# Kernel optimization log

Measured on AMD Instinct MI355X. Metric: run time of the kernel, lower is better.

## Reference

```python
import jax, jax.numpy as jnp
import numpy as np

ALPHA = 0.7
BETTA = 0.3
EPS = 1e-8


def _unit(v):
    n = jnp.linalg.norm(v, axis=-1, keepdims=True)
    return v / jnp.where(n > 0, n, 1.0)


def setup_inputs() -> dict:
    key = jax.random.key(0)
    k1, k2 = jax.random.split(key)
    N, D = 2097152, 3
    vec_1 = jax.random.normal(k1, (N, D), dtype=jnp.float32)
    vec_2 = jax.random.normal(k2, (N, D), dtype=jnp.float32)
    return {"vec_1": vec_1, "vec_2": vec_2}


def reference(vec_1, vec_2):
    # Row mask: keep rows where ||vec_1|| > 1e-8. Instead of boolean gather
    # (data-dependent shape), weight rows by the mask and divide by the count.
    norm1 = jnp.linalg.norm(vec_1, axis=-1, keepdims=True)  # [N,1]
    mask = (norm1 > EPS).astype(vec_1.dtype)                # [N,1]

    n1 = _unit(vec_1)                                       # [N,3]
    u2 = _unit(vec_2)
    # angle between vec_1 and vec_2 (RotationVectors.angle)
    cos_sim = jnp.clip(jnp.sum(n1 * u2, axis=-1), -1.0, 1.0)  # [N]
    a = jnp.arccos(cos_sim)
    # orthonormal companion: Gram-Schmidt of vec_2 against n1
    n2 = _unit(vec_2 - n1 * jnp.sum(n1 * vec_2, axis=-1, keepdims=True))

    sin_a = jnp.sin(a)[:, None]            # [N,1]
    cos_a_m1 = (jnp.cos(a) - 1.0)[:, None]  # [N,1]

    # bmm(M, ones) is just the row-sum of M. For M = x yT the row-sum is
    # x * sum(y), so we never materialize the [N,3,3] outer products:
    s1 = jnp.sum(n1, axis=-1, keepdims=True)  # [N,1]
    s2 = jnp.sum(n2, axis=-1, keepdims=True)
    u_ta = sin_a * (n2 * s1 - n1 * s2)        # transform_a @ ones, [N,3]
    u_tb = cos_a_m1 * (n1 * s1 + n2 * s2)     # transform_b @ ones, [N,3]
    # I @ ones == ones, so mse(I@ones, ones) == 0 elementwise.
    per_row = ALPHA * u_ta ** 2 + BETTA * u_tb ** 2  # [N,3]

    cnt = jnp.maximum(jnp.sum(mask), 1.0)
    loss = jnp.sum(per_row * mask, axis=0) / cnt     # mean over kept rows -> [3]
    return jnp.nan_to_num(loss, nan=0.0, posinf=0.1, neginf=-0.1)
```

## Files before the change

### kernel.cpp

```cpp
#include <hip/hip_runtime.h>
#include <math.h>

#define ALPHA 0.7f
#define BETTA 0.3f
#define EPS   1e-8f

#define BLOCK 256
#define ROWS_PER_THREAD 4
#define TILE_ROWS (BLOCK * ROWS_PER_THREAD)
#define TILE_F4   (TILE_ROWS * 3 / 4)

__device__ __forceinline__ void row_contrib(float x1, float y1, float z1,
                                            float x2, float y2, float z2,
                                            float& a0, float& a1, float& a2,
                                            float& ac) {
    float q1 = x1 * x1 + y1 * y1 + z1 * z1;
    float m = (q1 > EPS * EPS) ? 1.0f : 0.0f;
    float inv1 = (q1 > 0.0f) ? rsqrtf(q1) : 0.0f;
    float n1x = x1 * inv1, n1y = y1 * inv1, n1z = z1 * inv1;

    float q2 = x2 * x2 + y2 * y2 + z2 * z2;
    float inv2 = (q2 > 0.0f) ? rsqrtf(q2) : 0.0f;
    float u2x = x2 * inv2, u2y = y2 * inv2, u2z = z2 * inv2;

    float c = n1x * u2x + n1y * u2y + n1z * u2z;
    c = fminf(1.0f, fmaxf(-1.0f, c));
    float sin_a = sqrtf(fmaxf(0.0f, 1.0f - c * c));
    float cm1 = c - 1.0f;

    float d = n1x * x2 + n1y * y2 + n1z * z2;
    float wx = x2 - n1x * d, wy = y2 - n1y * d, wz = z2 - n1z * d;
    float wq = wx * wx + wy * wy + wz * wz;
    float invw = (wq > 0.0f) ? rsqrtf(wq) : 0.0f;
    float n2x = wx * invw, n2y = wy * invw, n2z = wz * invw;

    float s1 = n1x + n1y + n1z;
    float s2 = n2x + n2y + n2z;

    float tax = sin_a * (n2x * s1 - n1x * s2);
    float tay = sin_a * (n2y * s1 - n1y * s2);
    float taz = sin_a * (n2z * s1 - n1z * s2);

    float tbx = cm1 * (n1x * s1 + n2x * s2);
    float tby = cm1 * (n1y * s1 + n2y * s2);
    float tbz = cm1 * (n1z * s1 + n2z * s2);

    a0 += (ALPHA * tax * tax + BETTA * tbx * tbx) * m;
    a1 += (ALPHA * tay * tay + BETTA * tby * tby) * m;
    a2 += (ALPHA * taz * taz + BETTA * tbz * tbz) * m;
    ac += m;
}

__global__ __launch_bounds__(BLOCK) void trl_reduce(const float* __restrict__ v1,
                                                    const float* __restrict__ v2,
                                                    float4* __restrict__ ws,
                                                    int n_rows) {
    __shared__ float4 ldsA[TILE_F4];
    __shared__ float4 ldsB[TILE_F4];

    int t = threadIdx.x;
    long tile_row0 = (long)blockIdx.x * TILE_ROWS;

    float a0 = 0.0f, a1 = 0.0f, a2 = 0.0f, ac = 0.0f;

    if (tile_row0 + TILE_ROWS <= n_rows) {
        const float4* g1 = (const float4*)v1;
        const float4* g2 = (const float4*)v2;
        long base = (long)blockIdx.x * TILE_F4;

        float4 la0 = g1[base + 0 * BLOCK + t];
        float4 la1 = g1[base + 1 * BLOCK + t];
        float4 la2 = g1[base + 2 * BLOCK + t];
        float4 lb0 = g2[base + 0 * BLOCK + t];
        float4 lb1 = g2[base + 1 * BLOCK + t];
        float4 lb2 = g2[base + 2 * BLOCK + t];

        ldsA[0 * BLOCK + t] = la0;
        ldsA[1 * BLOCK + t] = la1;
        ldsA[2 * BLOCK + t] = la2;
        ldsB[0 * BLOCK + t] = lb0;
        ldsB[1 * BLOCK + t] = lb1;
        ldsB[2 * BLOCK + t] = lb2;
        __syncthreads();

        float4 A0 = ldsA[3 * t + 0];
        float4 A1 = ldsA[3 * t + 1];
        float4 A2 = ldsA[3 * t + 2];
        float4 B0 = ldsB[3 * t + 0];
        float4 B1 = ldsB[3 * t + 1];
        float4 B2 = ldsB[3 * t + 2];

        row_contrib(A0.x, A0.y, A0.z, B0.x, B0.y, B0.z, a0, a1, a2, ac);
        row_contrib(A0.w, A1.x, A1.y, B0.w, B1.x, B1.y, a0, a1, a2, ac);
        row_contrib(A1.z, A1.w, A2.x, B1.z, B1.w, B2.x, a0, a1, a2, ac);
        row_contrib(A2.y, A2.z, A2.w, B2.y, B2.z, B2.w, a0, a1, a2, ac);
    } else {
        long row0 = tile_row0 + (long)t * ROWS_PER_THREAD;
        for (long r = row0; r < n_rows && r < row0 + ROWS_PER_THREAD; ++r) {
            const float* q1 = v1 + r * 3;
            const float* q2 = v2 + r * 3;
            row_contrib(q1[0], q1[1], q1[2], q2[0], q2[1], q2[2], a0, a1, a2, ac);
        }
    }

    for (int off = 32; off > 0; off >>= 1) {
        a0 += __shfl_down(a0, off, 64);
        a1 += __shfl_down(a1, off, 64);
        a2 += __shfl_down(a2, off, 64);
        ac += __shfl_down(ac, off, 64);
    }

    __shared__ float smem[4][4];
    int lane = t & 63;
    int wave = t >> 6;
    if (lane == 0) {
        smem[wave][0] = a0;
        smem[wave][1] = a1;
        smem[wave][2] = a2;
        smem[wave][3] = ac;
    }
    __syncthreads();
    if (t == 0) {
        float4 o;
        o.x = smem[0][0] + smem[1][0] + smem[2][0] + smem[3][0];
        o.y = smem[0][1] + smem[1][1] + smem[2][1] + smem[3][1];
        o.z = smem[0][2] + smem[1][2] + smem[2][2] + smem[3][2];
        o.w = smem[0][3] + smem[1][3] + smem[2][3] + smem[3][3];
        ws[blockIdx.x] = o;
    }
}

__global__ __launch_bounds__(256) void trl_final(const float4* __restrict__ ws,
                                                 float* __restrict__ out,
                                                 int nblocks) {
    float s0 = 0.0f, s1 = 0.0f, s2 = 0.0f, sc = 0.0f;
    for (int i = threadIdx.x; i < nblocks; i += 256) {
        float4 p = ws[i];
        s0 += p.x; s1 += p.y; s2 += p.z; sc += p.w;
    }
    for (int off = 32; off > 0; off >>= 1) {
        s0 += __shfl_down(s0, off, 64);
        s1 += __shfl_down(s1, off, 64);
        s2 += __shfl_down(s2, off, 64);
        sc += __shfl_down(sc, off, 64);
    }
    __shared__ float smem[4][4];
    int lane = threadIdx.x & 63;
    int wave = threadIdx.x >> 6;
    if (lane == 0) {
        smem[wave][0] = s0;
        smem[wave][1] = s1;
        smem[wave][2] = s2;
        smem[wave][3] = sc;
    }
    __syncthreads();
    if (threadIdx.x < 3) {
        float num = smem[0][threadIdx.x] + smem[1][threadIdx.x] +
                    smem[2][threadIdx.x] + smem[3][threadIdx.x];
        float cnt = smem[0][3] + smem[1][3] + smem[2][3] + smem[3][3];
        cnt = fmaxf(cnt, 1.0f);
        float v = num / cnt;
        if (isnan(v)) v = 0.0f;
        else if (isinf(v)) v = (v > 0.0f) ? 0.1f : -0.1f;
        out[threadIdx.x] = v;
    }
}

extern "C" void kernel_launch(void* const* d_in, const int* in_sizes, int n_in,
                              void* d_out, int out_size, void* d_ws, size_t ws_size,
                              hipStream_t stream) {
    const float* v1 = (const float*)d_in[0];
    const float* v2 = (const float*)d_in[1];
    float* out = (float*)d_out;
    float4* ws = (float4*)d_ws;

    int n_rows = in_sizes[0] / 3;

    int grid = (n_rows + TILE_ROWS - 1) / TILE_ROWS;

    trl_reduce<<<grid, BLOCK, 0, stream>>>(v1, v2, ws, n_rows);
    trl_final<<<1, 256, 0, stream>>>(ws, out, grid);
}
```

Before: 89.87 us.

## Use persistent blocks with double-buffered LDS tiles and register prefetch

Replaces the one-tile-per-block grid (2048 blocks) with a fixed grid of up to 512 blocks. Each block walks a contiguous range of tiles and prefetches the next tile into registers while the current tile is computed from a double-buffered LDS staging area. The aim is to hide global load latency and to cut the number of partial sums the final kernel has to reduce. In exchange, far fewer waves are in flight per CU to cover memory latency, and any tail rows are handled serially by block 0.

```diff
diff --git a/kernel.cpp b/kernel.cpp
--- a/kernel.cpp
+++ b/kernel.cpp
@@ -6,9 +6,10 @@
 #define EPS   1e-8f
 
 #define BLOCK 256
-#define ROWS_PER_THREAD 4
-#define TILE_ROWS (BLOCK * ROWS_PER_THREAD)
+#define RPT   4
+#define TILE_ROWS (BLOCK * RPT)
 #define TILE_F4   (TILE_ROWS * 3 / 4)
+#define NBLOCKS 512
 
 __device__ __forceinline__ void row_contrib(float x1, float y1, float z1,
                                             float x2, float y2, float z2,
@@ -54,49 +55,72 @@
 __global__ __launch_bounds__(BLOCK) void trl_reduce(const float* __restrict__ v1,
                                                     const float* __restrict__ v2,
                                                     float4* __restrict__ ws,
-                                                    int n_rows) {
-    __shared__ float4 ldsA[TILE_F4];
-    __shared__ float4 ldsB[TILE_F4];
+                                                    int n_rows, int n_tiles,
+                                                    int iters) {
+    __shared__ float4 ldsA[2][TILE_F4];
+    __shared__ float4 ldsB[2][TILE_F4];
+    __shared__ float smem[4][4];
 
     int t = threadIdx.x;
-    long tile_row0 = (long)blockIdx.x * TILE_ROWS;
+    const float4* g1 = (const float4*)v1;
+    const float4* g2 = (const float4*)v2;
+
+    long tile0 = (long)blockIdx.x * iters;
+    int my_tiles = 0;
+    if (tile0 < n_tiles) {
+        long rem = (long)n_tiles - tile0;
+        my_tiles = (rem < iters) ? (int)rem : iters;
+    }
 
     float a0 = 0.0f, a1 = 0.0f, a2 = 0.0f, ac = 0.0f;
-
-    if (tile_row0 + TILE_ROWS <= n_rows) {
-        const float4* g1 = (const float4*)v1;
-        const float4* g2 = (const float4*)v2;
-        long base = (long)blockIdx.x * TILE_F4;
-
-        float4 la0 = g1[base + 0 * BLOCK + t];
-        float4 la1 = g1[base + 1 * BLOCK + t];
-        float4 la2 = g1[base + 2 * BLOCK + t];
-        float4 lb0 = g2[base + 0 * BLOCK + t];
-        float4 lb1 = g2[base + 1 * BLOCK + t];
-        float4 lb2 = g2[base + 2 * BLOCK + t];
-
-        ldsA[0 * BLOCK + t] = la0;
-        ldsA[1 * BLOCK + t] = la1;
-        ldsA[2 * BLOCK + t] = la2;
-        ldsB[0 * BLOCK + t] = lb0;
-        ldsB[1 * BLOCK + t] = lb1;
-        ldsB[2 * BLOCK + t] = lb2;
+    float4 ra[3], rb[3];
+
+    if (my_tiles > 0) {
+        long base = tile0 * TILE_F4;
+#pragma unroll
+        for (int j = 0; j < 3; ++j) ra[j] = g1[base + j * BLOCK + t];
+#pragma unroll
+        for (int j = 0; j < 3; ++j) rb[j] = g2[base + j * BLOCK + t];
+#pragma unroll
+        for (int j = 0; j < 3; ++j) ldsA[0][j * BLOCK + t] = ra[j];
+#pragma unroll
+        for (int j = 0; j < 3; ++j) ldsB[0][j * BLOCK + t] = rb[j];
+    }
+
+    for (int k = 0; k < my_tiles; ++k) {
+        int cur = k & 1;
+        if (k + 1 < my_tiles) {
+            long base = (tile0 + k + 1) * TILE_F4;
+#pragma unroll
+            for (int j = 0; j < 3; ++j) ra[j] = g1[base + j * BLOCK + t];
+#pragma unroll
+            for (int j = 0; j < 3; ++j) rb[j] = g2[base + j * BLOCK + t];
+        }
         __syncthreads();
 
-        float4 A0 = ldsA[3 * t + 0];
-        float4 A1 = ldsA[3 * t + 1];
-        float4 A2 = ldsA[3 * t + 2];
-        float4 B0 = ldsB[3 * t + 0];
-        float4 B1 = ldsB[3 * t + 1];
-        float4 B2 = ldsB[3 * t + 2];
+        float4 A0 = ldsA[cur][3 * t + 0];
+        float4 A1 = ldsA[cur][3 * t + 1];
+        float4 A2 = ldsA[cur][3 * t + 2];
+        float4 B0 = ldsB[cur][3 * t + 0];
+        float4 B1 = ldsB[cur][3 * t + 1];
+        float4 B2 = ldsB[cur][3 * t + 2];
 
         row_contrib(A0.x, A0.y, A0.z, B0.x, B0.y, B0.z, a0, a1, a2, ac);
         row_contrib(A0.w, A1.x, A1.y, B0.w, B1.x, B1.y, a0, a1, a2, ac);
         row_contrib(A1.z, A1.w, A2.x, B1.z, B1.w, B2.x, a0, a1, a2, ac);
         row_contrib(A2.y, A2.z, A2.w, B2.y, B2.z, B2.w, a0, a1, a2, ac);
-    } else {
-        long row0 = tile_row0 + (long)t * ROWS_PER_THREAD;
-        for (long r = row0; r < n_rows && r < row0 + ROWS_PER_THREAD; ++r) {
+
+        if (k + 1 < my_tiles) {
+            int nxt = cur ^ 1;
+#pragma unroll
+            for (int j = 0; j < 3; ++j) ldsA[nxt][j * BLOCK + t] = ra[j];
+#pragma unroll
+            for (int j = 0; j < 3; ++j) ldsB[nxt][j * BLOCK + t] = rb[j];
+        }
+    }
+
+    if (blockIdx.x == 0) {
+        for (long r = (long)n_tiles * TILE_ROWS + t; r < n_rows; r += BLOCK) {
             const float* q1 = v1 + r * 3;
             const float* q2 = v2 + r * 3;
             row_contrib(q1[0], q1[1], q1[2], q2[0], q2[1], q2[2], a0, a1, a2, ac);
@@ -110,9 +134,9 @@
         ac += __shfl_down(ac, off, 64);
     }
 
-    __shared__ float smem[4][4];
     int lane = t & 63;
     int wave = t >> 6;
+    __syncthreads();
     if (lane == 0) {
         smem[wave][0] = a0;
         smem[wave][1] = a1;
@@ -175,9 +199,10 @@
     float4* ws = (float4*)d_ws;
 
     int n_rows = in_sizes[0] / 3;
-
-    int grid = (n_rows + TILE_ROWS - 1) / TILE_ROWS;
-
-    trl_reduce<<<grid, BLOCK, 0, stream>>>(v1, v2, ws, n_rows);
+    int n_tiles = n_rows / TILE_ROWS;
+    int grid = (n_tiles < NBLOCKS) ? (n_tiles > 0 ? n_tiles : 1) : NBLOCKS;
+    int iters = (n_tiles + grid - 1) / grid;
+
+    trl_reduce<<<grid, BLOCK, 0, stream>>>(v1, v2, ws, n_rows, n_tiles, iters);
     trl_final<<<1, 256, 0, stream>>>(ws, out, grid);
 }
```

Result: slower. 101.3 us (+12.7%).

## Load tiles directly into LDS and emit per-wave partials

Applied to the files above, without the earlier changes.

Global-to-register-to-LDS staging is replaced with the global_load_lds builtin, which writes 16-byte vectors straight into shared memory. The block-level LDS reduction and its second barrier are removed, so each wave writes its own partial sum and the final kernel reduces four times as many entries. Tail rows are now handled by block 0 in a strided loop instead of a per-block fallback. The direct-to-LDS path depends on the 16-byte size being supported on this target and on the lane-to-address mapping being correct.

```diff
diff --git a/kernel.cpp b/kernel.cpp
--- a/kernel.cpp
+++ b/kernel.cpp
@@ -6,9 +6,14 @@
 #define EPS   1e-8f
 
 #define BLOCK 256
-#define ROWS_PER_THREAD 4
-#define TILE_ROWS (BLOCK * ROWS_PER_THREAD)
+#define RPT   4
+#define TILE_ROWS (BLOCK * RPT)
 #define TILE_F4   (TILE_ROWS * 3 / 4)
+
+typedef const __attribute__((address_space(1))) void* gas_ptr;
+typedef __attribute__((address_space(3))) void* las_ptr;
+#define GLOAD_LDS16(gp, lp) \
+    __builtin_amdgcn_global_load_lds((gas_ptr)(gp), (las_ptr)(lp), 16, 0, 0)
 
 __device__ __forceinline__ void row_contrib(float x1, float y1, float z1,
                                             float x2, float y2, float z2,
@@ -54,33 +59,32 @@
 __global__ __launch_bounds__(BLOCK) void trl_reduce(const float* __restrict__ v1,
                                                     const float* __restrict__ v2,
                                                     float4* __restrict__ ws,
-                                                    int n_rows) {
+                                                    int n_rows, int n_tiles) {
     __shared__ float4 ldsA[TILE_F4];
     __shared__ float4 ldsB[TILE_F4];
 
     int t = threadIdx.x;
-    long tile_row0 = (long)blockIdx.x * TILE_ROWS;
+    int lane = t & 63;
+    int w = t >> 6;
 
     float a0 = 0.0f, a1 = 0.0f, a2 = 0.0f, ac = 0.0f;
 
-    if (tile_row0 + TILE_ROWS <= n_rows) {
+    bool full = (blockIdx.x < (unsigned)n_tiles);
+    if (full) {
         const float4* g1 = (const float4*)v1;
         const float4* g2 = (const float4*)v2;
         long base = (long)blockIdx.x * TILE_F4;
+        int wslot = (w << 6);
 
-        float4 la0 = g1[base + 0 * BLOCK + t];
-        float4 la1 = g1[base + 1 * BLOCK + t];
-        float4 la2 = g1[base + 2 * BLOCK + t];
-        float4 lb0 = g2[base + 0 * BLOCK + t];
-        float4 lb1 = g2[base + 1 * BLOCK + t];
-        float4 lb2 = g2[base + 2 * BLOCK + t];
+#pragma unroll
+        for (int j = 0; j < 3; ++j)
+            GLOAD_LDS16(g1 + base + j * BLOCK + wslot + lane,
+                        &ldsA[j * BLOCK + wslot]);
+#pragma unroll
+        for (int j = 0; j < 3; ++j)
+            GLOAD_LDS16(g2 + base + j * BLOCK + wslot + lane,
+                        &ldsB[j * BLOCK + wslot]);
 
-        ldsA[0 * BLOCK + t] = la0;
-        ldsA[1 * BLOCK + t] = la1;
-        ldsA[2 * BLOCK + t] = la2;
-        ldsB[0 * BLOCK + t] = lb0;
-        ldsB[1 * BLOCK + t] = lb1;
-        ldsB[2 * BLOCK + t] = lb2;
         __syncthreads();
 
         float4 A0 = ldsA[3 * t + 0];
@@ -94,9 +98,10 @@
         row_contrib(A0.w, A1.x, A1.y, B0.w, B1.x, B1.y, a0, a1, a2, ac);
         row_contrib(A1.z, A1.w, A2.x, B1.z, B1.w, B2.x, a0, a1, a2, ac);
         row_contrib(A2.y, A2.z, A2.w, B2.y, B2.z, B2.w, a0, a1, a2, ac);
-    } else {
-        long row0 = tile_row0 + (long)t * ROWS_PER_THREAD;
-        for (long r = row0; r < n_rows && r < row0 + ROWS_PER_THREAD; ++r) {
+    }
+
+    if (blockIdx.x == 0) {
+        for (long r = (long)n_tiles * TILE_ROWS + t; r < n_rows; r += BLOCK) {
             const float* q1 = v1 + r * 3;
             const float* q2 = v2 + r * 3;
             row_contrib(q1[0], q1[1], q1[2], q2[0], q2[1], q2[2], a0, a1, a2, ac);
@@ -109,32 +114,18 @@
         a2 += __shfl_down(a2, off, 64);
         ac += __shfl_down(ac, off, 64);
     }
-
-    __shared__ float smem[4][4];
-    int lane = t & 63;
-    int wave = t >> 6;
     if (lane == 0) {
-        smem[wave][0] = a0;
-        smem[wave][1] = a1;
-        smem[wave][2] = a2;
-        smem[wave][3] = ac;
-    }
-    __syncthreads();
-    if (t == 0) {
         float4 o;
-        o.x = smem[0][0] + smem[1][0] + smem[2][0] + smem[3][0];
-        o.y = smem[0][1] + smem[1][1] + smem[2][1] + smem[3][1];
-        o.z = smem[0][2] + smem[1][2] + smem[2][2] + smem[3][2];
-        o.w = smem[0][3] + smem[1][3] + smem[2][3] + smem[3][3];
-        ws[blockIdx.x] = o;
+        o.x = a0; o.y = a1; o.z = a2; o.w = ac;
+        ws[(size_t)blockIdx.x * 4 + w] = o;
     }
 }
 
 __global__ __launch_bounds__(256) void trl_final(const float4* __restrict__ ws,
                                                  float* __restrict__ out,
-                                                 int nblocks) {
+                                                 int nparts) {
     float s0 = 0.0f, s1 = 0.0f, s2 = 0.0f, sc = 0.0f;
-    for (int i = threadIdx.x; i < nblocks; i += 256) {
+    for (int i = threadIdx.x; i < nparts; i += 256) {
         float4 p = ws[i];
         s0 += p.x; s1 += p.y; s2 += p.z; sc += p.w;
     }
@@ -175,9 +166,9 @@
     float4* ws = (float4*)d_ws;
 
     int n_rows = in_sizes[0] / 3;
+    int n_tiles = n_rows / TILE_ROWS;
+    int grid = (n_tiles > 0) ? n_tiles : 1;
 
-    int grid = (n_rows + TILE_ROWS - 1) / TILE_ROWS;
-
-    trl_reduce<<<grid, BLOCK, 0, stream>>>(v1, v2, ws, n_rows);
-    trl_final<<<1, 256, 0, stream>>>(ws, out, grid);
+    trl_reduce<<<grid, BLOCK, 0, stream>>>(v1, v2, ws, n_rows, n_tiles);
+    trl_final<<<1, 256, 0, stream>>>(ws, out, grid * 4);
 }
```

Result: slower. 94.03 us (+4.6%).
